# Kernel optimization log

Hardware: AMD Instinct MI355X
Metric: run time of the kernel (lower is better)

Reference implementation:

```python
import jax, jax.numpy as jnp
import numpy as np

B, N, C = 4, 2048, 1024
H = 16
D = C // H  # head_size = 64


def setup_inputs() -> dict:
    key = jax.random.key(0)
    ks = jax.random.split(key, 9)
    s = 1.0 / np.sqrt(C)
    return {
        "x": jax.random.normal(ks[0], (B, N, C), dtype=jnp.float32),
        "Wq": jax.random.normal(ks[1], (C, C), dtype=jnp.float32) * s,
        "bq": jnp.zeros((C,), dtype=jnp.float32),
        "Wk": jax.random.normal(ks[2], (C, C), dtype=jnp.float32) * s,
        "bk": jnp.zeros((C,), dtype=jnp.float32),
        "Wv": jax.random.normal(ks[3], (C, C), dtype=jnp.float32) * s,
        "bv": jnp.zeros((C,), dtype=jnp.float32),
        "Wo": jax.random.normal(ks[4], (C, C), dtype=jnp.float32) * s,
        "bo": jnp.zeros((C,), dtype=jnp.float32),
    }


def reference(x, Wq, bq, Wk, bk, Wv, bv, Wo, bo):
    scale = 1.0 / np.sqrt(D).astype(np.float32)
    # projections: [B,N,C] -> [B,H,N,D]
    def split_heads(t):
        return t.reshape(B, N, H, D).transpose(0, 2, 1, 3)
    q = split_heads(x @ Wq + bq)
    k = split_heads(x @ Wk + bk)
    v = split_heads(x @ Wv + bv)
    # scores: [B,H,N,N] -- full NxN materialized as in the original module
    attn = jnp.einsum("bhqd,bhkd->bhqk", q, k) * scale
    attn = jax.nn.softmax(attn, axis=-1)
    # context: [B,H,N,D] -> [B,N,C]
    ctx = jnp.einsum("bhqk,bhkd->bhqd", attn, v)
    ctx = ctx.transpose(0, 2, 1, 3).reshape(B, N, C)
    return ctx @ Wo + bo
```

## Files before the change

### kernel.cpp

```cpp
#include <hip/hip_runtime.h>
#include <hip/hip_bf16.h>

typedef __bf16 bf16_t;
typedef __bf16 bf16x4 __attribute__((ext_vector_type(4)));
typedef __bf16 bf16x8 __attribute__((ext_vector_type(8)));
typedef float f32x4 __attribute__((ext_vector_type(4)));
typedef unsigned int u32;

#define B_ 4
#define N_ 2048
#define C_ 1024
#define H_ 16
#define D_ 64

#define MFMA32(a, b, c) __builtin_amdgcn_mfma_f32_16x16x32_bf16((a), (b), (c), 0, 0, 0)

#if __has_builtin(__builtin_amdgcn_exp2f)
#define EXP2F(x) __builtin_amdgcn_exp2f(x)
#else
#define EXP2F(x) __expf((x) * 0.6931471805599453f)
#endif

#define QSCALE 0.18033688011112042f

__device__ __forceinline__ void async16(const bf16_t* g, bf16_t* l) {
    __builtin_amdgcn_global_load_lds(
        (const u32 __attribute__((address_space(1)))*)g,
        (u32 __attribute__((address_space(3)))*)l, 16, 0, 0);
}

#define SBAR()  asm volatile("s_barrier" ::: "memory")
#define VM4()   asm volatile("s_waitcnt vmcnt(4)" ::: "memory")
#define VM0()   asm volatile("s_waitcnt vmcnt(0)" ::: "memory")

__global__ __launch_bounds__(256)
void xconv_kernel(const float* __restrict__ x, bf16_t* __restrict__ xb)
{
    const size_t i = ((size_t)blockIdx.x * 256 + threadIdx.x) * 8;
    float4 a = *(const float4*)(x + i);
    float4 b = *(const float4*)(x + i + 4);
    bf16x8 o;
    o[0] = (bf16_t)a.x; o[1] = (bf16_t)a.y; o[2] = (bf16_t)a.z; o[3] = (bf16_t)a.w;
    o[4] = (bf16_t)b.x; o[5] = (bf16_t)b.y; o[6] = (bf16_t)b.z; o[7] = (bf16_t)b.w;
    *(bf16x8*)(xb + i) = o;
}

__global__ __launch_bounds__(256)
void wtrans_kernel(const float* __restrict__ W0, const float* __restrict__ W1,
                   const float* __restrict__ W2, const float* __restrict__ W3,
                   bf16_t* __restrict__ T0, bf16_t* __restrict__ T1,
                   bf16_t* __restrict__ T2, bf16_t* __restrict__ T3)
{
    const float* W; bf16_t* T;
    switch (blockIdx.z) {
        case 0:  W = W0; T = T0; break;
        case 1:  W = W1; T = T1; break;
        case 2:  W = W2; T = T2; break;
        default: W = W3; T = T3; break;
    }
    __shared__ bf16_t tile[64 * 72];
    const int tid = threadIdx.x;
    const int r0 = blockIdx.y * 64;
    const int c0 = blockIdx.x * 64;

    const int rr = tid >> 4;
    const int cc = (tid & 15) * 4;
    #pragma unroll
    for (int i = 0; i < 4; ++i) {
        const int row = rr + i * 16;
        float4 v = *(const float4*)(W + (size_t)(r0 + row) * C_ + c0 + cc);
        tile[(cc + 0) * 72 + row] = (bf16_t)v.x;
        tile[(cc + 1) * 72 + row] = (bf16_t)v.y;
        tile[(cc + 2) * 72 + row] = (bf16_t)v.z;
        tile[(cc + 3) * 72 + row] = (bf16_t)v.w;
    }
    __syncthreads();
    #pragma unroll
    for (int i = 0; i < 2; ++i) {
        const int ch = i * 256 + tid;
        const int n  = ch >> 3;
        const int k8 = (ch & 7) * 8;
        bf16x8 o = *(const bf16x8*)&tile[n * 72 + k8];
        *(bf16x8*)(T + (size_t)(c0 + n) * C_ + r0 + k8) = o;
    }
}


__device__ __forceinline__ void mfma16(f32x4 (&acc)[8][4], const bf16x8 (&af)[4],
                                       const bf16x8 (&bfv)[4], int mf0)
{
    #pragma unroll
    for (int i = 0; i < 4; ++i)
        #pragma unroll
        for (int j = 0; j < 4; ++j)
            acc[mf0 + i][j] = MFMA32(af[i], bfv[j], acc[mf0 + i][j]);
}

__global__ __launch_bounds__(512) __attribute__((amdgpu_waves_per_eu(2, 2)))
void gemm_qkv_kernel(const bf16_t* __restrict__ A, const bf16_t* __restrict__ Wt,
                     const float* __restrict__ bq, const float* __restrict__ bk,
                     const float* __restrict__ bv,
                     bf16_t* __restrict__ Qb, bf16_t* __restrict__ Kb,
                     bf16_t* __restrict__ Vtb)
{
    __shared__ bf16_t smem[65536];

    const int tid  = threadIdx.x;
    const int w    = tid >> 6;
    const int lane = tid & 63;
    const int c    = lane & 15;
    const int quad = lane >> 4;
    const int wr   = w >> 2;
    const int wc   = w & 3;

    const int bid = blockIdx.x;
    const int x8  = bid & 7;
    const int ii  = bid >> 3;
    const int mb  = x8 * 4 + (ii & 3);
    const int nb  = ii >> 2;
    const int m0  = mb * 256, n0 = nb * 256;

    const int r0s = tid >> 2;
    const int kc  = (tid & 3) ^ (r0s & 3);
    const bf16_t* Ast0 = A  + (size_t)(m0 + r0s) * C_ + kc * 8;
    const bf16_t* Ast1 = A  + (size_t)(m0 + r0s + 128) * C_ + kc * 8;
    const bf16_t* Bst0 = Wt + (size_t)(n0 + r0s) * C_ + kc * 8;
    const bf16_t* Bst1 = Wt + (size_t)(n0 + r0s + 128) * C_ + kc * 8;

    const int xorc = (quad ^ (c & 3)) * 8;
    const bf16_t* Ard = smem + (wr * 128 + c) * 32 + xorc;
    const bf16_t* Brd = smem + 32768 + (wc * 64 + c) * 32 + xorc;
    bf16_t* sAB = smem + w * 512;

#define STAGE_A(BUF, KS, KOFF) do { \
    async16(Ast0 + (KOFF), sAB + (BUF) * 16384 + (KS) * 8192); \
    async16(Ast1 + (KOFF), sAB + (BUF) * 16384 + (KS) * 8192 + 4096); } while (0)
#define STAGE_B(BUF, KS, KOFF) do { \
    async16(Bst0 + (KOFF), sAB + 32768 + (BUF) * 16384 + (KS) * 8192); \
    async16(Bst1 + (KOFF), sAB + 32768 + (BUF) * 16384 + (KS) * 8192 + 4096); } while (0)
#define LD4A(BUF, KS, HALF) do { \
    af[0] = *(const bf16x8*)(Ard + (BUF) * 16384 + (KS) * 8192 + (HALF) * 2048); \
    af[1] = *(const bf16x8*)(Ard + (BUF) * 16384 + (KS) * 8192 + (HALF) * 2048 + 512); \
    af[2] = *(const bf16x8*)(Ard + (BUF) * 16384 + (KS) * 8192 + (HALF) * 2048 + 1024); \
    af[3] = *(const bf16x8*)(Ard + (BUF) * 16384 + (KS) * 8192 + (HALF) * 2048 + 1536); } while (0)
#define LD4B(BUF, KS) do { \
    bfv[0] = *(const bf16x8*)(Brd + (BUF) * 16384 + (KS) * 8192); \
    bfv[1] = *(const bf16x8*)(Brd + (BUF) * 16384 + (KS) * 8192 + 512); \
    bfv[2] = *(const bf16x8*)(Brd + (BUF) * 16384 + (KS) * 8192 + 1024); \
    bfv[3] = *(const bf16x8*)(Brd + (BUF) * 16384 + (KS) * 8192 + 1536); } while (0)

#define TILE(CUR, DOSTAGE) do { \
    LD4A(CUR, 0, 0); LD4B(CUR, 0); \
    if (DOSTAGE) STAGE_A(1 - (CUR), 0, 64); \
    SBAR(); \
    __builtin_amdgcn_s_setprio(1); mfma16(acc, af, bfv, 0); __builtin_amdgcn_s_setprio(0); \
    SBAR(); \
    LD4A(CUR, 0, 1); \
    if (DOSTAGE) STAGE_B(1 - (CUR), 0, 64); \
    SBAR(); \
    __builtin_amdgcn_s_setprio(1); mfma16(acc, af, bfv, 4); __builtin_amdgcn_s_setprio(0); \
    if (DOSTAGE) VM4(); else VM0(); \
    SBAR(); \
    LD4A(CUR, 1, 1); LD4B(CUR, 1); \
    if (DOSTAGE) STAGE_A(1 - (CUR), 1, 96); \
    SBAR(); \
    __builtin_amdgcn_s_setprio(1); mfma16(acc, af, bfv, 4); __builtin_amdgcn_s_setprio(0); \
    SBAR(); \
    LD4A(CUR, 1, 0); \
    if (DOSTAGE) STAGE_B(1 - (CUR), 1, 96); \
    SBAR(); \
    __builtin_amdgcn_s_setprio(1); mfma16(acc, af, bfv, 0); __builtin_amdgcn_s_setprio(0); \
    if (DOSTAGE) { VM4(); Ast0 += 64; Ast1 += 64; Bst0 += 64; Bst1 += 64; } \
    SBAR(); \
} while (0)

    f32x4 acc[8][4] = {};
    bf16x8 af[4], bfv[4];

    STAGE_A(0, 0, 0);
    STAGE_B(0, 0, 0);
    STAGE_A(0, 1, 32);
    STAGE_B(0, 1, 32);
    VM4();
    SBAR();

    #pragma unroll 1
    for (int tt = 0; tt < 7; ++tt) {
        TILE(0, 1);
        TILE(1, 1);
    }
    TILE(0, 1);
    TILE(1, 0);

#undef TILE
#undef LD4A
#undef LD4B
#undef STAGE_A
#undef STAGE_B

    const int which = n0 >> 10;
    const float* bias = (which == 0) ? bq : (which == 1) ? bk : bv;

    #pragma unroll
    for (int nf = 0; nf < 4; ++nf) {
        const int col  = n0 + wc * 64 + nf * 16 + c;
        const int ncol = col & 1023;
        const float bsf = bias[ncol];
        const int h = ncol >> 6, d = ncol & 63;
        #pragma unroll
        for (int mf = 0; mf < 8; ++mf) {
            const int rbase = m0 + wr * 128 + mf * 16 + quad * 4;
            if (which < 2) {
                bf16_t* out = which ? Kb : Qb;
                const float sc = which ? 1.0f : QSCALE;
                #pragma unroll
                for (int r = 0; r < 4; ++r) {
                    const int row = rbase + r;
                    const int bb = row >> 11, n = row & 2047;
                    out[(((size_t)bb * H_ + h) * N_ + n) * D_ + d] =
                        (bf16_t)((acc[mf][nf][r] + bsf) * sc);
                }
            } else {
                const int bb = rbase >> 11, nbv = rbase & 2047;
                bf16x4 o;
                #pragma unroll
                for (int r = 0; r < 4; ++r) o[r] = (bf16_t)(acc[mf][nf][r] + bsf);
                *(bf16x4*)(Vtb + (((size_t)bb * H_ + h) * D_ + d) * N_ + nbv) = o;
            }
        }
    }
}

__global__ __launch_bounds__(256)
void gemm_out_kernel(const bf16_t* __restrict__ A, const bf16_t* __restrict__ Bt,
                     const float* __restrict__ bias, float* __restrict__ out)
{
    __shared__ bf16_t As[2][128 * 32];
    __shared__ bf16_t Bs[2][128 * 32];

    const int tid  = threadIdx.x;
    const int w    = tid >> 6;
    const int lane = tid & 63;
    const int c    = lane & 15;
    const int quad = lane >> 4;
    const int n0   = blockIdx.x * 128;
    const int m0   = blockIdx.y * 128;
    const int wm   = (w & 1) * 64;
    const int wn   = (w >> 1) * 64;

    f32x4 acc[4][4] = {};

    for (int k0 = 0; k0 < C_; k0 += 64) {
        __syncthreads();
        #pragma unroll
        for (int hh = 0; hh < 2; ++hh) {
            #pragma unroll
            for (int ph = 0; ph < 2; ++ph) {
                const int ch  = ph * 256 + tid;
                const int row = ch >> 2;
                const int k8  = (ch & 3) * 8;
                const int wbase = (ph * 256 + w * 64) * 8;
                async16(A  + (size_t)(m0 + row) * C_ + k0 + hh * 32 + k8, &As[hh][wbase]);
                async16(Bt + (size_t)(n0 + row) * C_ + k0 + hh * 32 + k8, &Bs[hh][wbase]);
            }
        }
        __syncthreads();

        bf16x8 af[2][4], bfr[2][4];
        #pragma unroll
        for (int hh = 0; hh < 2; ++hh) {
            #pragma unroll
            for (int mf = 0; mf < 4; ++mf)
                af[hh][mf] = *(const bf16x8*)&As[hh][(wm + mf * 16 + c) * 32 + quad * 8];
            #pragma unroll
            for (int nf = 0; nf < 4; ++nf)
                bfr[hh][nf] = *(const bf16x8*)&Bs[hh][(wn + nf * 16 + c) * 32 + quad * 8];
        }

        #pragma unroll
        for (int mf = 0; mf < 4; ++mf)
            #pragma unroll
            for (int nf = 0; nf < 4; ++nf) {
                acc[mf][nf] = MFMA32(af[0][mf], bfr[0][nf], acc[mf][nf]);
                acc[mf][nf] = MFMA32(af[1][mf], bfr[1][nf], acc[mf][nf]);
            }
    }

    #pragma unroll
    for (int nf = 0; nf < 4; ++nf) {
        const int col   = n0 + wn + nf * 16 + c;
        const float bsf = bias[col];
        #pragma unroll
        for (int mf = 0; mf < 4; ++mf) {
            const int rbase = m0 + wm + mf * 16 + quad * 4;
            #pragma unroll
            for (int r = 0; r < 4; ++r)
                out[(size_t)(rbase + r) * C_ + col] = acc[mf][nf][r] + bsf;
        }
    }
}

__global__ __launch_bounds__(256, 2)
void attn_kernel(const bf16_t* __restrict__ Q, const bf16_t* __restrict__ K,
                 const bf16_t* __restrict__ Vt, bf16_t* __restrict__ ctx)
{
    __shared__ bf16_t ksh[64 * 64];
    __shared__ bf16_t vsh[64 * 64];

    const int tid  = threadIdx.x;
    const int w    = tid >> 6;
    const int lane = tid & 63;
    const int c    = lane & 15;
    const int quad = lane >> 4;

    const int bid   = blockIdx.x;
    const int bh    = (bid & 7) * 8 + ((bid >> 3) & 7);
    const int qtile = bid >> 6;
    const int b = bh >> 4, h = bh & 15;
    const size_t base = (size_t)bh * N_ * D_;
    const int qb = qtile * 256 + w * 64;

    bf16x8 qf[4][2];
    #pragma unroll
    for (int g = 0; g < 4; ++g)
        #pragma unroll
        for (int hh = 0; hh < 2; ++hh)
            qf[g][hh] = *(const bf16x8*)(Q + base + (size_t)(qb + g * 16 + c) * D_ + hh * 32 + quad * 8);

    bf16x8 ones;
    #pragma unroll
    for (int j = 0; j < 8; ++j) ones[j] = (bf16_t)1.0f;

    f32x4 O[4][4] = {};
    f32x4 O5[4] = {};

    for (int kt = 0; kt < N_; kt += 64) {
        __syncthreads();
        #pragma unroll
        for (int ph = 0; ph < 2; ++ph) {
            const int ch = ph * 256 + tid;
            const int rr = ch >> 3;
            const int e8 = ch & 7;
            const int sw = (e8 ^ (rr & 7)) * 8;
            bf16x8 kv = *(const bf16x8*)(K  + base + (size_t)(kt + rr) * D_ + e8 * 8);
            *(bf16x8*)&ksh[rr * 64 + sw] = kv;
            bf16x8 vv = *(const bf16x8*)(Vt + base + (size_t)rr * N_ + kt + e8 * 8);
            *(bf16x8*)&vsh[rr * 64 + sw] = vv;
        }
        __syncthreads();

        #pragma unroll
        for (int ss = 0; ss < 2; ++ss) {
            bf16x8 kb[2][2];
            #pragma unroll
            for (int s2 = 0; s2 < 2; ++s2) {
                const int key = (ss * 2 + s2) * 16 + c;
                #pragma unroll
                for (int hh = 0; hh < 2; ++hh)
                    kb[s2][hh] = *(const bf16x8*)&ksh[key * 64 + (((hh * 4 + quad) ^ (c & 7)) * 8)];
            }
            bf16x8 va[4];
            const int k8lo = ss * 4 + (quad >> 1);
            const int half = (quad & 1) * 4;
            #pragma unroll
            for (int df = 0; df < 4; ++df) {
                const int row = (df * 16 + c) * 64;
                bf16x4 lo = *(const bf16x4*)&vsh[row + ((k8lo       ^ (c & 7)) * 8) + half];
                bf16x4 hi = *(const bf16x4*)&vsh[row + (((k8lo + 2) ^ (c & 7)) * 8) + half];
                #pragma unroll
                for (int j = 0; j < 4; ++j) { va[df][j] = lo[j]; va[df][4 + j] = hi[j]; }
            }

            #pragma unroll
            for (int g = 0; g < 4; ++g) {
                f32x4 s0 = {}, s1 = {};
                s0 = MFMA32(kb[0][0], qf[g][0], s0);
                s0 = MFMA32(kb[0][1], qf[g][1], s0);
                s1 = MFMA32(kb[1][0], qf[g][0], s1);
                s1 = MFMA32(kb[1][1], qf[g][1], s1);

                bf16x8 pb;
                #pragma unroll
                for (int r = 0; r < 4; ++r) {
                    pb[r]     = (bf16_t)EXP2F(s0[r]);
                    pb[4 + r] = (bf16_t)EXP2F(s1[r]);
                }

                #pragma unroll
                for (int df = 0; df < 4; ++df)
                    O[g][df] = MFMA32(va[df], pb, O[g][df]);
                O5[g] = MFMA32(ones, pb, O5[g]);
            }
        }
    }

    #pragma unroll
    for (int g = 0; g < 4; ++g) {
        const float inv_l = 1.0f / O5[g][0];
        const int q = qb + g * 16 + c;
        #pragma unroll
        for (int df = 0; df < 4; ++df) {
            bf16x4 o;
            #pragma unroll
            for (int r = 0; r < 4; ++r) o[r] = (bf16_t)(O[g][df][r] * inv_l);
            *(bf16x4*)(ctx + ((size_t)b * N_ + q) * C_ + h * 64 + df * 16 + quad * 4) = o;
        }
    }
}

extern "C" void kernel_launch(void* const* d_in, const int* in_sizes, int n_in,
                              void* d_out, int out_size, void* d_ws, size_t ws_size,
                              hipStream_t stream) {
    const float* x  = (const float*)d_in[0];
    const float* Wq = (const float*)d_in[1];
    const float* bq = (const float*)d_in[2];
    const float* Wk = (const float*)d_in[3];
    const float* bk = (const float*)d_in[4];
    const float* Wv = (const float*)d_in[5];
    const float* bv = (const float*)d_in[6];
    const float* Wo = (const float*)d_in[7];
    const float* bo = (const float*)d_in[8];

    bf16_t* ws = (bf16_t*)d_ws;
    const size_t per = (size_t)B_ * N_ * C_;
    bf16_t* xb  = ws;
    bf16_t* ctx = ws;
    bf16_t* Qb  = ws + per;
    bf16_t* Kb  = ws + 2 * per;
    bf16_t* Vtb = ws + 3 * per;
    bf16_t* Wtqkv = ws + 4 * per;
    bf16_t* Wtq = Wtqkv;
    bf16_t* Wtk = Wtqkv + (size_t)C_ * C_;
    bf16_t* Wtv = Wtqkv + 2 * (size_t)C_ * C_;
    bf16_t* Wto = Wtqkv + 3 * (size_t)C_ * C_;

    dim3 blk(256);

    xconv_kernel<<<dim3(per / 2048), blk, 0, stream>>>(x, xb);
    wtrans_kernel<<<dim3(16, 16, 4), blk, 0, stream>>>(Wq, Wk, Wv, Wo, Wtq, Wtk, Wtv, Wto);

    gemm_qkv_kernel<<<dim3(384), dim3(512), 0, stream>>>(xb, Wtqkv, bq, bk, bv, Qb, Kb, Vtb);

    attn_kernel<<<dim3(512), blk, 0, stream>>>(Qb, Kb, Vtb, ctx);

    gemm_out_kernel<<<dim3(8, 64), blk, 0, stream>>>(ctx, Wto, bo, (float*)d_out);
}
```

Before: 273.9 us.

## Share a triple-buffered 128x256 GEMM core between QKV and output projections

Moves the GEMM mainloop into a shared device function with a 128x256 block tile, three-stage LDS buffering (six async loads per stage, waitcnt 6), and 8 waves. The QKV projection now launches 768 smaller-tile blocks instead of 384 256x256 blocks and drops the waves-per-eu attribute. The output projection replaces its simple double-synced 128x128 loop with the same pipelined core. The aim is better load/compute overlap and more blocks across CUs, at the cost of more LDS per block and more reloading of the B operand.

```diff
diff --git a/kernel.cpp b/kernel.cpp
--- a/kernel.cpp
+++ b/kernel.cpp
@@ -30,7 +30,7 @@
 }
 
 #define SBAR()  asm volatile("s_barrier" ::: "memory")
-#define VM4()   asm volatile("s_waitcnt vmcnt(4)" ::: "memory")
+#define VM6()   asm volatile("s_waitcnt vmcnt(6)" ::: "memory")
 #define VM0()   asm volatile("s_waitcnt vmcnt(0)" ::: "memory")
 
 __global__ __launch_bounds__(256)
@@ -85,26 +85,11 @@
     }
 }
 
-
-__device__ __forceinline__ void mfma16(f32x4 (&acc)[8][4], const bf16x8 (&af)[4],
-                                       const bf16x8 (&bfv)[4], int mf0)
-{
-    #pragma unroll
-    for (int i = 0; i < 4; ++i)
-        #pragma unroll
-        for (int j = 0; j < 4; ++j)
-            acc[mf0 + i][j] = MFMA32(af[i], bfv[j], acc[mf0 + i][j]);
-}
-
-__global__ __launch_bounds__(512) __attribute__((amdgpu_waves_per_eu(2, 2)))
-void gemm_qkv_kernel(const bf16_t* __restrict__ A, const bf16_t* __restrict__ Wt,
-                     const float* __restrict__ bq, const float* __restrict__ bk,
-                     const float* __restrict__ bv,
-                     bf16_t* __restrict__ Qb, bf16_t* __restrict__ Kb,
-                     bf16_t* __restrict__ Vtb)
-{
-    __shared__ bf16_t smem[65536];
-
+__device__ __forceinline__ void gemm128x256(const bf16_t* __restrict__ A,
+                                            const bf16_t* __restrict__ Bt,
+                                            bf16_t* smem, int m0, int n0,
+                                            f32x4 (&acc)[4][4])
+{
     const int tid  = threadIdx.x;
     const int w    = tid >> 6;
     const int lane = tid & 63;
@@ -113,90 +98,106 @@
     const int wr   = w >> 2;
     const int wc   = w & 3;
 
-    const int bid = blockIdx.x;
-    const int x8  = bid & 7;
-    const int ii  = bid >> 3;
-    const int mb  = x8 * 4 + (ii & 3);
-    const int nb  = ii >> 2;
-    const int m0  = mb * 256, n0 = nb * 256;
-
     const int r0s = tid >> 2;
     const int kc  = (tid & 3) ^ (r0s & 3);
     const bf16_t* Ast0 = A  + (size_t)(m0 + r0s) * C_ + kc * 8;
-    const bf16_t* Ast1 = A  + (size_t)(m0 + r0s + 128) * C_ + kc * 8;
-    const bf16_t* Bst0 = Wt + (size_t)(n0 + r0s) * C_ + kc * 8;
-    const bf16_t* Bst1 = Wt + (size_t)(n0 + r0s + 128) * C_ + kc * 8;
+    const bf16_t* Bst0 = Bt + (size_t)(n0 + r0s) * C_ + kc * 8;
+    const bf16_t* Bst1 = Bt + (size_t)(n0 + r0s + 128) * C_ + kc * 8;
 
     const int xorc = (quad ^ (c & 3)) * 8;
-    const bf16_t* Ard = smem + (wr * 128 + c) * 32 + xorc;
-    const bf16_t* Brd = smem + 32768 + (wc * 64 + c) * 32 + xorc;
-    bf16_t* sAB = smem + w * 512;
-
-#define STAGE_A(BUF, KS, KOFF) do { \
-    async16(Ast0 + (KOFF), sAB + (BUF) * 16384 + (KS) * 8192); \
-    async16(Ast1 + (KOFF), sAB + (BUF) * 16384 + (KS) * 8192 + 4096); } while (0)
-#define STAGE_B(BUF, KS, KOFF) do { \
-    async16(Bst0 + (KOFF), sAB + 32768 + (BUF) * 16384 + (KS) * 8192); \
-    async16(Bst1 + (KOFF), sAB + 32768 + (BUF) * 16384 + (KS) * 8192 + 4096); } while (0)
-#define LD4A(BUF, KS, HALF) do { \
-    af[0] = *(const bf16x8*)(Ard + (BUF) * 16384 + (KS) * 8192 + (HALF) * 2048); \
-    af[1] = *(const bf16x8*)(Ard + (BUF) * 16384 + (KS) * 8192 + (HALF) * 2048 + 512); \
-    af[2] = *(const bf16x8*)(Ard + (BUF) * 16384 + (KS) * 8192 + (HALF) * 2048 + 1024); \
-    af[3] = *(const bf16x8*)(Ard + (BUF) * 16384 + (KS) * 8192 + (HALF) * 2048 + 1536); } while (0)
-#define LD4B(BUF, KS) do { \
+    const bf16_t* Ard = smem + (wr * 64 + c) * 32 + xorc;
+    const bf16_t* Brd = smem + 24576 + (wc * 64 + c) * 32 + xorc;
+    bf16_t* sw = smem + w * 512;
+
+    bf16x8 af[4], bfv[4];
+
+#define STAGE6(BUF, KOFF) do { \
+    async16(Ast0 + (KOFF),      sw + (BUF) * 8192); \
+    async16(Ast0 + (KOFF) + 32, sw + (BUF) * 8192 + 4096); \
+    async16(Bst0 + (KOFF),      sw + 24576 + (BUF) * 16384); \
+    async16(Bst1 + (KOFF),      sw + 24576 + (BUF) * 16384 + 4096); \
+    async16(Bst0 + (KOFF) + 32, sw + 24576 + (BUF) * 16384 + 8192); \
+    async16(Bst1 + (KOFF) + 32, sw + 24576 + (BUF) * 16384 + 12288); } while (0)
+
+#define LDFRAGS(BUF, KS) do { \
+    af[0]  = *(const bf16x8*)(Ard + (BUF) * 8192 + (KS) * 4096); \
+    af[1]  = *(const bf16x8*)(Ard + (BUF) * 8192 + (KS) * 4096 + 512); \
+    af[2]  = *(const bf16x8*)(Ard + (BUF) * 8192 + (KS) * 4096 + 1024); \
+    af[3]  = *(const bf16x8*)(Ard + (BUF) * 8192 + (KS) * 4096 + 1536); \
     bfv[0] = *(const bf16x8*)(Brd + (BUF) * 16384 + (KS) * 8192); \
     bfv[1] = *(const bf16x8*)(Brd + (BUF) * 16384 + (KS) * 8192 + 512); \
     bfv[2] = *(const bf16x8*)(Brd + (BUF) * 16384 + (KS) * 8192 + 1024); \
     bfv[3] = *(const bf16x8*)(Brd + (BUF) * 16384 + (KS) * 8192 + 1536); } while (0)
 
-#define TILE(CUR, DOSTAGE) do { \
-    LD4A(CUR, 0, 0); LD4B(CUR, 0); \
-    if (DOSTAGE) STAGE_A(1 - (CUR), 0, 64); \
+#define MFMA16() do { \
+    _Pragma("unroll") \
+    for (int i = 0; i < 4; ++i) \
+        _Pragma("unroll") \
+        for (int j = 0; j < 4; ++j) \
+            acc[i][j] = MFMA32(af[i], bfv[j], acc[i][j]); } while (0)
+
+#define TILE(BUF, NXT, DOSTAGE, KOFF, VMK) do { \
+    if (DOSTAGE) STAGE6(NXT, KOFF); \
+    LDFRAGS(BUF, 0); \
     SBAR(); \
-    __builtin_amdgcn_s_setprio(1); mfma16(acc, af, bfv, 0); __builtin_amdgcn_s_setprio(0); \
+    __builtin_amdgcn_s_setprio(1); MFMA16(); __builtin_amdgcn_s_setprio(0); \
     SBAR(); \
-    LD4A(CUR, 0, 1); \
-    if (DOSTAGE) STAGE_B(1 - (CUR), 0, 64); \
+    LDFRAGS(BUF, 1); \
     SBAR(); \
-    __builtin_amdgcn_s_setprio(1); mfma16(acc, af, bfv, 4); __builtin_amdgcn_s_setprio(0); \
-    if (DOSTAGE) VM4(); else VM0(); \
-    SBAR(); \
-    LD4A(CUR, 1, 1); LD4B(CUR, 1); \
-    if (DOSTAGE) STAGE_A(1 - (CUR), 1, 96); \
-    SBAR(); \
-    __builtin_amdgcn_s_setprio(1); mfma16(acc, af, bfv, 4); __builtin_amdgcn_s_setprio(0); \
-    SBAR(); \
-    LD4A(CUR, 1, 0); \
-    if (DOSTAGE) STAGE_B(1 - (CUR), 1, 96); \
-    SBAR(); \
-    __builtin_amdgcn_s_setprio(1); mfma16(acc, af, bfv, 0); __builtin_amdgcn_s_setprio(0); \
-    if (DOSTAGE) { VM4(); Ast0 += 64; Ast1 += 64; Bst0 += 64; Bst1 += 64; } \
+    __builtin_amdgcn_s_setprio(1); MFMA16(); __builtin_amdgcn_s_setprio(0); \
+    VMK; \
     SBAR(); \
 } while (0)
 
-    f32x4 acc[8][4] = {};
-    bf16x8 af[4], bfv[4];
-
-    STAGE_A(0, 0, 0);
-    STAGE_B(0, 0, 0);
-    STAGE_A(0, 1, 32);
-    STAGE_B(0, 1, 32);
-    VM4();
+    STAGE6(0, 0);
+    STAGE6(1, 64);
+    VM6();
     SBAR();
 
     #pragma unroll 1
-    for (int tt = 0; tt < 7; ++tt) {
-        TILE(0, 1);
-        TILE(1, 1);
-    }
-    TILE(0, 1);
-    TILE(1, 0);
+    for (int tt = 0; tt < 4; ++tt) {
+        TILE(0, 2, 1, 128, VM6());
+        TILE(1, 0, 1, 192, VM6());
+        TILE(2, 1, 1, 256, VM6());
+        Ast0 += 192; Bst0 += 192; Bst1 += 192;
+    }
+    TILE(0, 2, 1, 128, VM6());
+    TILE(1, 0, 1, 192, VM6());
+    TILE(2, 1, 0, 0,   VM0());
+    TILE(0, 0, 0, 0,   ((void)0));
 
 #undef TILE
-#undef LD4A
-#undef LD4B
-#undef STAGE_A
-#undef STAGE_B
+#undef MFMA16
+#undef LDFRAGS
+#undef STAGE6
+}
+
+__global__ __launch_bounds__(512)
+void gemm_qkv_kernel(const bf16_t* __restrict__ A, const bf16_t* __restrict__ Wt,
+                     const float* __restrict__ bq, const float* __restrict__ bk,
+                     const float* __restrict__ bv,
+                     bf16_t* __restrict__ Qb, bf16_t* __restrict__ Kb,
+                     bf16_t* __restrict__ Vtb)
+{
+    __shared__ bf16_t smem[73728];
+
+    const int bid = blockIdx.x;
+    const int x8  = bid & 7;
+    const int ii  = bid >> 3;
+    const int mb  = x8 * 8 + (ii & 7);
+    const int nb  = ii >> 3;
+    const int m0  = mb * 128, n0 = nb * 256;
+
+    f32x4 acc[4][4] = {};
+    gemm128x256(A, Wt, smem, m0, n0, acc);
+
+    const int tid  = threadIdx.x;
+    const int w    = tid >> 6;
+    const int lane = tid & 63;
+    const int c    = lane & 15;
+    const int quad = lane >> 4;
+    const int wr   = w >> 2;
+    const int wc   = w & 3;
 
     const int which = n0 >> 10;
     const float* bias = (which == 0) ? bq : (which == 1) ? bk : bv;
@@ -208,8 +209,8 @@
         const float bsf = bias[ncol];
         const int h = ncol >> 6, d = ncol & 63;
         #pragma unroll
-        for (int mf = 0; mf < 8; ++mf) {
-            const int rbase = m0 + wr * 128 + mf * 16 + quad * 4;
+        for (int mf = 0; mf < 4; ++mf) {
+            const int rbase = m0 + wr * 64 + mf * 16 + quad * 4;
             if (which < 2) {
                 bf16_t* out = which ? Kb : Qb;
                 const float sc = which ? 1.0f : QSCALE;
@@ -231,68 +232,37 @@
     }
 }
 
-__global__ __launch_bounds__(256)
+__global__ __launch_bounds__(512)
 void gemm_out_kernel(const bf16_t* __restrict__ A, const bf16_t* __restrict__ Bt,
                      const float* __restrict__ bias, float* __restrict__ out)
 {
-    __shared__ bf16_t As[2][128 * 32];
-    __shared__ bf16_t Bs[2][128 * 32];
+    __shared__ bf16_t smem[73728];
+
+    const int bid = blockIdx.x;
+    const int x8  = bid & 7;
+    const int ii  = bid >> 3;
+    const int mb  = x8 * 8 + (ii & 7);
+    const int nb  = ii >> 3;
+    const int m0  = mb * 128, n0 = nb * 256;
+
+    f32x4 acc[4][4] = {};
+    gemm128x256(A, Bt, smem, m0, n0, acc);
 
     const int tid  = threadIdx.x;
     const int w    = tid >> 6;
     const int lane = tid & 63;
     const int c    = lane & 15;
     const int quad = lane >> 4;
-    const int n0   = blockIdx.x * 128;
-    const int m0   = blockIdx.y * 128;
-    const int wm   = (w & 1) * 64;
-    const int wn   = (w >> 1) * 64;
-
-    f32x4 acc[4][4] = {};
-
-    for (int k0 = 0; k0 < C_; k0 += 64) {
-        __syncthreads();
-        #pragma unroll
-        for (int hh = 0; hh < 2; ++hh) {
-            #pragma unroll
-            for (int ph = 0; ph < 2; ++ph) {
-                const int ch  = ph * 256 + tid;
-                const int row = ch >> 2;
-                const int k8  = (ch & 3) * 8;
-                const int wbase = (ph * 256 + w * 64) * 8;
-                async16(A  + (size_t)(m0 + row) * C_ + k0 + hh * 32 + k8, &As[hh][wbase]);
-                async16(Bt + (size_t)(n0 + row) * C_ + k0 + hh * 32 + k8, &Bs[hh][wbase]);
-            }
-        }
-        __syncthreads();
-
-        bf16x8 af[2][4], bfr[2][4];
-        #pragma unroll
-        for (int hh = 0; hh < 2; ++hh) {
-            #pragma unroll
-            for (int mf = 0; mf < 4; ++mf)
-                af[hh][mf] = *(const bf16x8*)&As[hh][(wm + mf * 16 + c) * 32 + quad * 8];
-            #pragma unroll
-            for (int nf = 0; nf < 4; ++nf)
-                bfr[hh][nf] = *(const bf16x8*)&Bs[hh][(wn + nf * 16 + c) * 32 + quad * 8];
-        }
-
-        #pragma unroll
-        for (int mf = 0; mf < 4; ++mf)
-            #pragma unroll
-            for (int nf = 0; nf < 4; ++nf) {
-                acc[mf][nf] = MFMA32(af[0][mf], bfr[0][nf], acc[mf][nf]);
-                acc[mf][nf] = MFMA32(af[1][mf], bfr[1][nf], acc[mf][nf]);
-            }
-    }
+    const int wr   = w >> 2;
+    const int wc   = w & 3;
 
     #pragma unroll
     for (int nf = 0; nf < 4; ++nf) {
-        const int col   = n0 + wn + nf * 16 + c;
+        const int col   = n0 + wc * 64 + nf * 16 + c;
         const float bsf = bias[col];
         #pragma unroll
         for (int mf = 0; mf < 4; ++mf) {
-            const int rbase = m0 + wm + mf * 16 + quad * 4;
+            const int rbase = m0 + wr * 64 + mf * 16 + quad * 4;
             #pragma unroll
             for (int r = 0; r < 4; ++r)
                 out[(size_t)(rbase + r) * C_ + col] = acc[mf][nf][r] + bsf;
@@ -439,9 +409,9 @@
     xconv_kernel<<<dim3(per / 2048), blk, 0, stream>>>(x, xb);
     wtrans_kernel<<<dim3(16, 16, 4), blk, 0, stream>>>(Wq, Wk, Wv, Wo, Wtq, Wtk, Wtv, Wto);
 
-    gemm_qkv_kernel<<<dim3(384), dim3(512), 0, stream>>>(xb, Wtqkv, bq, bk, bv, Qb, Kb, Vtb);
+    gemm_qkv_kernel<<<dim3(768), dim3(512), 0, stream>>>(xb, Wtqkv, bq, bk, bv, Qb, Kb, Vtb);
 
     attn_kernel<<<dim3(512), blk, 0, stream>>>(Qb, Kb, Vtb, ctx);
 
-    gemm_out_kernel<<<dim3(8, 64), blk, 0, stream>>>(ctx, Wto, bo, (float*)d_out);
-}
+    gemm_out_kernel<<<dim3(256), dim3(512), 0, stream>>>(ctx, Wto, bo, (float*)d_out);
+}
```

Result: faster. 262.9 us (-4.0%).
